# Performance work log

Hardware: AMD Instinct MI355X
Metric: run time of the kernel (lower is better)

The kernel has to match this reference:

```python
import jax, jax.numpy as jnp
import numpy as np

H = 16; W = 16; C_IN = 32; RNN_IN = 64; HID = 128; OUT = 512; B = 512


def _upsample_bilinear_ac(x, oh, ow):
    """Bilinear upsample with align_corners=True (matches nn.UpsamplingBilinear2d). x: (B,C,h,w)."""
    h, w = x.shape[2], x.shape[3]
    ys = (jnp.arange(oh, dtype=jnp.float32) * (h - 1) / (oh - 1))
    y0 = jnp.floor(ys).astype(jnp.int32)
    y1 = jnp.minimum(y0 + 1, h - 1)
    wy = (ys - y0.astype(jnp.float32))[None, None, :, None]
    xs = (jnp.arange(ow, dtype=jnp.float32) * (w - 1) / (ow - 1))
    x0 = jnp.floor(xs).astype(jnp.int32)
    x1 = jnp.minimum(x0 + 1, w - 1)
    wx = (xs - x0.astype(jnp.float32))[None, None, None, :]
    rows = x[:, :, y0, :] * (1.0 - wy) + x[:, :, y1, :] * wy  # (B,C,oh,w)
    out = rows[:, :, :, x0] * (1.0 - wx) + rows[:, :, :, x1] * wx  # (B,C,oh,ow)
    return out


def setup_inputs() -> dict:
    key = jax.random.key(0)
    ks = jax.random.split(key, 8)
    def winit(k, shape, fan_in):
        return jax.random.normal(k, shape, jnp.float32) / np.float32(np.sqrt(fan_in))
    return {
        "x": jax.random.normal(ks[0], (B, C_IN, H, W), jnp.float32),
        "h0": jax.random.normal(ks[1], (B, HID), jnp.float32),
        "W_in": winit(ks[2], (RNN_IN, C_IN), C_IN),
        "b_in": jnp.zeros((RNN_IN,), jnp.float32),
        "W_ih": winit(ks[3], (HID, RNN_IN), RNN_IN),
        "b_ih": jnp.zeros((HID,), jnp.float32),
        "W_hh": winit(ks[4], (HID, HID), HID),
        "b_hh": jnp.zeros((HID,), jnp.float32),
        "W_out": winit(ks[5], (OUT, HID), HID),
        "b_out": jnp.zeros((OUT,), jnp.float32),
    }


def reference(x, h0, W_in, b_in, W_ih, b_ih, W_hh, b_hh, W_out, b_out):
    b = x.shape[0]
    # (B,C,H,W) -> (B,L,C), L = H*W raster order
    x_seq = x.transpose(0, 2, 3, 1).reshape(b, H * W, C_IN)
    proj = x_seq @ W_in.T + b_in                      # (B,L,RNN_IN)
    pre = proj @ W_ih.T + b_ih                        # (B,L,HID), input part of RNNCell precomputed

    def step(h, p_t):
        h_new = jnp.tanh(p_t + h @ W_hh.T + b_hh)
        return h_new, h_new

    _, hs = jax.lax.scan(step, h0, pre.transpose(1, 0, 2))  # (L,B,HID)
    hs_map = hs.reshape(H, W, b, HID).transpose(2, 3, 0, 1)  # (B,HID,H,W)
    up = _upsample_bilinear_ac(hs_map, 2 * H, 2 * W)         # (B,HID,32,32)
    act = up * jnp.clip(up + 3.0, 0.0, 6.0) * (1.0 / 6.0)    # hardswish
    pooled = act.mean(axis=(2, 3))                           # (B,HID)
    return pooled @ W_out.T + b_out
```

## Files before the change

### kernel.cpp

```cpp
#include <hip/hip_runtime.h>

#define L 256
#define BATCH 512
#define CIN 32
#define HIDN 128
#define OUTN 512

typedef _Float16 f16x8 __attribute__((ext_vector_type(8)));
typedef float f32x4 __attribute__((ext_vector_type(4)));

#define MFMA16(a, b, c) __builtin_amdgcn_mfma_f32_16x16x32_f16(a, b, c, 0, 0, 0)

static __device__ __forceinline__ unsigned short f16b(_Float16 h) {
    unsigned short u; __builtin_memcpy(&u, &h, 2); return u;
}


__global__ __launch_bounds__(256) void prep_kernel(
    const float* __restrict__ W_in, const float* __restrict__ b_in,
    const float* __restrict__ W_ih, const float* __restrict__ b_ih,
    const float* __restrict__ b_hh, const float* __restrict__ Whh,
    unsigned short* __restrict__ Wh, unsigned short* __restrict__ Wl,
    unsigned short* __restrict__ Wch, unsigned short* __restrict__ Wcl,
    float* __restrict__ bpre)
{
    const int tid = threadIdx.x;
    __shared__ float win[64 * CIN];
    for (int i = tid; i < 64 * CIN; i += 256) win[i] = W_in[i];
    __syncthreads();
    if (tid < 128) {
        const int j = tid;
        float acc[CIN];
#pragma unroll
        for (int c = 0; c < CIN; ++c) acc[c] = 0.f;
        float bs = b_ih[j] + b_hh[j];
        for (int m = 0; m < 64; ++m) {
            float w = W_ih[j * 64 + m];
            bs += w * b_in[m];
#pragma unroll
            for (int c = 0; c < CIN; ++c) acc[c] += w * win[m * CIN + c];
        }
        bpre[j] = bs;
#pragma unroll
        for (int c = 0; c < CIN; ++c) {
            _Float16 h = (_Float16)acc[c];
            _Float16 l = (_Float16)(acc[c] - (float)h);
            Wch[j * CIN + c] = f16b(h);
            Wcl[j * CIN + c] = f16b(l);
        }
    } else {
        const int j = tid - 128;
        for (int k = 0; k < HIDN; k += 4) {
            float4 v = *(const float4*)(Whh + j * HIDN + k);
            float vv[4] = {v.x, v.y, v.z, v.w};
#pragma unroll
            for (int u = 0; u < 4; ++u) {
                _Float16 h = (_Float16)vv[u];
                _Float16 l = (_Float16)(vv[u] - (float)h);
                Wh[j * HIDN + k + u] = f16b(h);
                Wl[j * HIDN + k + u] = f16b(l);
            }
        }
    }
}

__global__ __launch_bounds__(512, 1) void rnn_kernel(
    const float* __restrict__ x, const float* __restrict__ h0,
    const unsigned short* __restrict__ Wh, const unsigned short* __restrict__ Wl,
    const unsigned short* __restrict__ Wch, const unsigned short* __restrict__ Wcl,
    const float* __restrict__ bpre, unsigned short* __restrict__ hs)
{
    const int tid = threadIdx.x;
    const int bb = blockIdx.x;
    const int lane = tid & 63;
    const int w = tid >> 6;
    const int n = lane & 15;
    const int q = lane >> 4;

    __shared__ unsigned short hbuf[2][16][HIDN];
    __shared__ unsigned short xc[2][16][16][CIN];

    f16x8 Ah[4], Al[4], Axh, Axl;
    const int jr = w * 16 + n;
#pragma unroll
    for (int kc = 0; kc < 4; ++kc) {
        Ah[kc] = *(const f16x8*)(Wh + jr * HIDN + kc * 32 + q * 8);
        Al[kc] = *(const f16x8*)(Wl + jr * HIDN + kc * 32 + q * 8);
    }
    Axh = *(const f16x8*)(Wch + jr * CIN + q * 8);
    Axl = *(const f16x8*)(Wcl + jr * CIN + q * 8);
    float4 bv = *(const float4*)(bpre + w * 16 + q * 4);
    f32x4 bp = (f32x4){bv.x, bv.y, bv.z, bv.w};

    if (tid < 256) {
        const int ni = tid >> 4, gi = tid & 15;
        const float4* src = (const float4*)(h0 + ((size_t)bb * 16 + ni) * HIDN + gi * 8);
        float4 a = src[0], b4 = src[1];
        float vv[8] = {a.x, a.y, a.z, a.w, b4.x, b4.y, b4.z, b4.w};
        unsigned short o[8];
#pragma unroll
        for (int i = 0; i < 8; ++i) o[i] = f16b((_Float16)vv[i]);
        *(uint4*)&hbuf[0][ni][(gi ^ (ni & 7)) * 8] = *(uint4*)o;
    }

    float4 xr[4];
    auto issue_chunk = [&](int ci) {
#pragma unroll
        for (int r = 0; r < 4; ++r) {
            int i = tid + r * 512;
            int nn = i >> 7, cc = (i >> 2) & 31, tq = i & 3;
            xr[r] = *(const float4*)(x + (((size_t)bb * 16 + nn) * CIN + cc) * L + ci * 16 + tq * 4);
        }
    };
    auto write_chunk = [&](int buf) {
#pragma unroll
        for (int r = 0; r < 4; ++r) {
            int i = tid + r * 512;
            int nn = i >> 7, cc = (i >> 2) & 31, tq = i & 3;
            float vv[4] = {xr[r].x, xr[r].y, xr[r].z, xr[r].w};
#pragma unroll
            for (int k = 0; k < 4; ++k)
                xc[buf][tq * 4 + k][nn][cc] = f16b((_Float16)vv[k]);
        }
    };

    issue_chunk(0);
    write_chunk(0);
    issue_chunk(1);
    __syncthreads();

    unsigned short* hsp = hs + ((size_t)bb * 16 + n) * HIDN + w * 16 + q * 4;

    for (int t = 0; t < L; ++t) {
        const int p = t & 1;
        const int cb = (t >> 4) & 1, tt = t & 15;

        f16x8 Bh[4];
#pragma unroll
        for (int kc = 0; kc < 4; ++kc)
            Bh[kc] = *(const f16x8*)&hbuf[p][n][((4 * kc + q) ^ (n & 7)) * 8];
        f16x8 xB = *(const f16x8*)&xc[cb][tt][n][q * 8];

        f32x4 aH = bp;
        f32x4 aL = (f32x4){0.f, 0.f, 0.f, 0.f};
#pragma unroll
        for (int kc = 0; kc < 4; ++kc) {
            aH = MFMA16(Ah[kc], Bh[kc], aH);
            aL = MFMA16(Al[kc], Bh[kc], aL);
        }
        aH = MFMA16(Axh, xB, aH);
        aL = MFMA16(Axl, xB, aL);

        if (tt == 15 && t < L - 16) {
            write_chunk(cb ^ 1);
            if (t < L - 32) issue_chunk((t >> 4) + 2);
        }

        f32x4 acc = aH + aL;
        unsigned short o[4];
#pragma unroll
        for (int r = 0; r < 4; ++r) {
            float e = __expf(2.f * acc[r]);
            float hv = 1.f - 2.f * __builtin_amdgcn_rcpf(e + 1.f);
            o[r] = f16b((_Float16)hv);
        }
        uint2 pk; __builtin_memcpy(&pk, o, 8);
        const int G = (w * 2 + (q >> 1)) ^ (n & 7);
        *(uint2*)&hbuf[p ^ 1][n][G * 8 + (q & 1) * 4] = pk;
        *(uint2*)(hsp + (size_t)t * (BATCH * HIDN)) = pk;

        asm volatile("" ::: "memory");
        __builtin_amdgcn_s_waitcnt(0xC07F);
        __builtin_amdgcn_s_barrier();
        asm volatile("" ::: "memory");
    }
}

__global__ __launch_bounds__(256) void pool_out_kernel(
    const unsigned short* __restrict__ hs, const float* __restrict__ W_out,
    const float* __restrict__ b_out, float* __restrict__ out)
{
    const int b = blockIdx.x, tid = threadIdx.x;
    __shared__ unsigned short m[L][HIDN];
    __shared__ float ps[2][HIDN];
    __shared__ float pooled_s[HIDN];

#pragma unroll
    for (int it = 0; it < 16; ++it) {
        int i = tid + it * 256;
        int t = i >> 4, g = i & 15;
        *(uint4*)&m[t][g * 8] =
            *(const uint4*)(hs + (size_t)t * (BATCH * HIDN) + b * HIDN + g * 8);
    }
    __syncthreads();

    const int jo = tid & 127, sub = tid >> 7;
    float acc = 0.f;
    for (int oy = sub * 16; oy < sub * 16 + 16; ++oy) {
        float ysf = oy * (15.f / 31.f);
        int y0 = (int)ysf; float wy = ysf - (float)y0; int y1 = min(y0 + 1, 15);
        float rb[16];
#pragma unroll
        for (int sx = 0; sx < 16; ++sx) {
            float v0 = (float)*(const _Float16*)&m[y0 * 16 + sx][jo];
            float v1 = (float)*(const _Float16*)&m[y1 * 16 + sx][jo];
            rb[sx] = v0 + wy * (v1 - v0);
        }
#pragma unroll
        for (int ox = 0; ox < 32; ++ox) {
            float xsf = ox * (15.f / 31.f);
            int x0 = (int)xsf; float wx = xsf - (float)x0; int x1 = min(x0 + 1, 15);
            float v = rb[x0] + wx * (rb[x1] - rb[x0]);
            float t6 = fminf(fmaxf(v + 3.f, 0.f), 6.f);
            acc += v * t6;
        }
    }
    ps[sub][jo] = acc;
    __syncthreads();
    if (tid < 128) pooled_s[tid] = (ps[0][tid] + ps[1][tid]) * (1.f / 6144.f);
    __syncthreads();

    for (int o = tid; o < OUTN; o += 256) {
        float a = b_out[o];
#pragma unroll 8
        for (int k = 0; k < HIDN; k += 4) {
            float4 wv = *(const float4*)(W_out + o * HIDN + k);
            float4 pv = *(const float4*)&pooled_s[k];
            a += wv.x * pv.x + wv.y * pv.y + wv.z * pv.z + wv.w * pv.w;
        }
        out[b * OUTN + o] = a;
    }
}

extern "C" void kernel_launch(void* const* d_in, const int* in_sizes, int n_in,
                              void* d_out, int out_size, void* d_ws, size_t ws_size,
                              hipStream_t stream)
{
    const float* x     = (const float*)d_in[0];
    const float* h0    = (const float*)d_in[1];
    const float* W_in  = (const float*)d_in[2];
    const float* b_in  = (const float*)d_in[3];
    const float* W_ih  = (const float*)d_in[4];
    const float* b_ih  = (const float*)d_in[5];
    const float* W_hh  = (const float*)d_in[6];
    const float* b_hh  = (const float*)d_in[7];
    const float* W_out = (const float*)d_in[8];
    const float* b_out = (const float*)d_in[9];
    float* out = (float*)d_out;

    char* wsb = (char*)d_ws;
    unsigned short* Wh  = (unsigned short*)(wsb);
    unsigned short* Wl  = (unsigned short*)(wsb + 32768);
    unsigned short* Wch = (unsigned short*)(wsb + 65536);
    unsigned short* Wcl = (unsigned short*)(wsb + 73728);
    float* bpre         = (float*)(wsb + 81920);
    unsigned short* hsb = (unsigned short*)(wsb + 98304);

    prep_kernel<<<1, 256, 0, stream>>>(W_in, b_in, W_ih, b_ih, b_hh, W_hh,
                                       Wh, Wl, Wch, Wcl, bpre);
    rnn_kernel<<<32, 512, 0, stream>>>(x, h0, Wh, Wl, Wch, Wcl, bpre, hsb);
    pool_out_kernel<<<512, 256, 0, stream>>>(hsb, W_out, b_out, out);
}
```

Baseline: 228.3 us.

## Pretranspose x to fp16 in prep kernel and shorten recurrent MFMA chain

Adds 32 extra blocks to the prep kernel that transpose x into a time-major fp16 layout in workspace. The RNN kernel can then fetch each step's input directly with a one-step-ahead register prefetch, replacing the shared-memory chunk staging that ran every 16 steps. The per-step MFMA dependency chain is split across four accumulators so the sequential recurrence has lower latency, and the loop is unrolled by two. The cost is an extra global round trip for x and a prefetch that reads one step past the end of the buffer.

New measurement: 245.1 us. +7.3%, slower.

```diff
diff --git a/kernel.cpp b/kernel.cpp
--- a/kernel.cpp
+++ b/kernel.cpp
@@ -17,14 +17,51 @@
 
 
 __global__ __launch_bounds__(256) void prep_kernel(
+    const float* __restrict__ x,
     const float* __restrict__ W_in, const float* __restrict__ b_in,
     const float* __restrict__ W_ih, const float* __restrict__ b_ih,
     const float* __restrict__ b_hh, const float* __restrict__ Whh,
     unsigned short* __restrict__ Wh, unsigned short* __restrict__ Wl,
     unsigned short* __restrict__ Wch, unsigned short* __restrict__ Wcl,
-    float* __restrict__ bpre)
+    float* __restrict__ bpre, unsigned short* __restrict__ xT)
 {
     const int tid = threadIdx.x;
+
+    if (blockIdx.x != 0) {
+        const int bb = blockIdx.x - 1;
+        __shared__ float tile[32][16][33];
+        const int wv = tid >> 6, l = tid & 63;
+        const int wn = l >> 2, wc0 = (l & 3) * 8;
+        for (int tc = 0; tc < 8; ++tc) {
+#pragma unroll
+            for (int r = 0; r < 16; ++r) {
+                int i = tid + r * 256;
+                int nn = i >> 8, cc = (i >> 3) & 31, tq = i & 7;
+                float4 v = *(const float4*)(
+                    x + ((size_t)(bb * 16 + nn) * CIN + cc) * L + tc * 32 + tq * 4);
+                int cs = cc ^ ((tq & 3) << 3);
+                tile[tq * 4 + 0][nn][cs] = v.x;
+                tile[tq * 4 + 1][nn][cs] = v.y;
+                tile[tq * 4 + 2][nn][cs] = v.z;
+                tile[tq * 4 + 3][nn][cs] = v.w;
+            }
+            __syncthreads();
+#pragma unroll
+            for (int it = 0; it < 8; ++it) {
+                int tl = wv + it * 4;
+                int swz = ((tl >> 2) & 3) << 3;
+                const float* src = &tile[tl][wn][wc0 ^ swz];
+                unsigned short o[8];
+#pragma unroll
+                for (int k = 0; k < 8; ++k) o[k] = f16b((_Float16)src[k]);
+                *(uint4*)(xT + ((size_t)(tc * 32 + tl) * BATCH + bb * 16 + wn) * CIN + wc0)
+                    = *(uint4*)o;
+            }
+            __syncthreads();
+        }
+        return;
+    }
+
     __shared__ float win[64 * CIN];
     for (int i = tid; i < 64 * CIN; i += 256) win[i] = W_in[i];
     __syncthreads();
@@ -44,9 +81,9 @@
 #pragma unroll
         for (int c = 0; c < CIN; ++c) {
             _Float16 h = (_Float16)acc[c];
-            _Float16 l = (_Float16)(acc[c] - (float)h);
+            _Float16 lo = (_Float16)(acc[c] - (float)h);
             Wch[j * CIN + c] = f16b(h);
-            Wcl[j * CIN + c] = f16b(l);
+            Wcl[j * CIN + c] = f16b(lo);
         }
     } else {
         const int j = tid - 128;
@@ -56,19 +93,20 @@
 #pragma unroll
             for (int u = 0; u < 4; ++u) {
                 _Float16 h = (_Float16)vv[u];
-                _Float16 l = (_Float16)(vv[u] - (float)h);
+                _Float16 lo = (_Float16)(vv[u] - (float)h);
                 Wh[j * HIDN + k + u] = f16b(h);
-                Wl[j * HIDN + k + u] = f16b(l);
+                Wl[j * HIDN + k + u] = f16b(lo);
             }
         }
     }
 }
 
 __global__ __launch_bounds__(512, 1) void rnn_kernel(
-    const float* __restrict__ x, const float* __restrict__ h0,
+    const float* __restrict__ h0,
     const unsigned short* __restrict__ Wh, const unsigned short* __restrict__ Wl,
     const unsigned short* __restrict__ Wch, const unsigned short* __restrict__ Wcl,
-    const float* __restrict__ bpre, unsigned short* __restrict__ hs)
+    const float* __restrict__ bpre, const unsigned short* __restrict__ xT,
+    unsigned short* __restrict__ hs)
 {
     const int tid = threadIdx.x;
     const int bb = blockIdx.x;
@@ -78,7 +116,6 @@
     const int q = lane >> 4;
 
     __shared__ unsigned short hbuf[2][16][HIDN];
-    __shared__ unsigned short xc[2][16][16][CIN];
 
     f16x8 Ah[4], Al[4], Axh, Axl;
     const int jr = w * 16 + n;
@@ -91,6 +128,11 @@
     Axl = *(const f16x8*)(Wcl + jr * CIN + q * 8);
     float4 bv = *(const float4*)(bpre + w * 16 + q * 4);
     f32x4 bp = (f32x4){bv.x, bv.y, bv.z, bv.w};
+    const f32x4 zero4 = (f32x4){0.f, 0.f, 0.f, 0.f};
+
+    const unsigned short* xp = xT + ((size_t)(bb * 16 + n) * CIN + q * 8);
+    f16x8 xb0, xb1;
+    xb0 = *(const f16x8*)(xp);
 
     if (tid < 256) {
         const int ni = tid >> 4, gi = tid & 15;
@@ -102,78 +144,50 @@
         for (int i = 0; i < 8; ++i) o[i] = f16b((_Float16)vv[i]);
         *(uint4*)&hbuf[0][ni][(gi ^ (ni & 7)) * 8] = *(uint4*)o;
     }
-
-    float4 xr[4];
-    auto issue_chunk = [&](int ci) {
-#pragma unroll
-        for (int r = 0; r < 4; ++r) {
-            int i = tid + r * 512;
-            int nn = i >> 7, cc = (i >> 2) & 31, tq = i & 3;
-            xr[r] = *(const float4*)(x + (((size_t)bb * 16 + nn) * CIN + cc) * L + ci * 16 + tq * 4);
-        }
-    };
-    auto write_chunk = [&](int buf) {
-#pragma unroll
-        for (int r = 0; r < 4; ++r) {
-            int i = tid + r * 512;
-            int nn = i >> 7, cc = (i >> 2) & 31, tq = i & 3;
-            float vv[4] = {xr[r].x, xr[r].y, xr[r].z, xr[r].w};
-#pragma unroll
-            for (int k = 0; k < 4; ++k)
-                xc[buf][tq * 4 + k][nn][cc] = f16b((_Float16)vv[k]);
-        }
-    };
-
-    issue_chunk(0);
-    write_chunk(0);
-    issue_chunk(1);
     __syncthreads();
 
     unsigned short* hsp = hs + ((size_t)bb * 16 + n) * HIDN + w * 16 + q * 4;
-
-    for (int t = 0; t < L; ++t) {
-        const int p = t & 1;
-        const int cb = (t >> 4) & 1, tt = t & 15;
-
-        f16x8 Bh[4];
-#pragma unroll
-        for (int kc = 0; kc < 4; ++kc)
-            Bh[kc] = *(const f16x8*)&hbuf[p][n][((4 * kc + q) ^ (n & 7)) * 8];
-        f16x8 xB = *(const f16x8*)&xc[cb][tt][n][q * 8];
-
-        f32x4 aH = bp;
-        f32x4 aL = (f32x4){0.f, 0.f, 0.f, 0.f};
-#pragma unroll
-        for (int kc = 0; kc < 4; ++kc) {
-            aH = MFMA16(Ah[kc], Bh[kc], aH);
-            aL = MFMA16(Al[kc], Bh[kc], aL);
-        }
-        aH = MFMA16(Axh, xB, aH);
-        aL = MFMA16(Axl, xB, aL);
-
-        if (tt == 15 && t < L - 16) {
-            write_chunk(cb ^ 1);
-            if (t < L - 32) issue_chunk((t >> 4) + 2);
-        }
-
-        f32x4 acc = aH + aL;
-        unsigned short o[4];
-#pragma unroll
-        for (int r = 0; r < 4; ++r) {
-            float e = __expf(2.f * acc[r]);
-            float hv = 1.f - 2.f * __builtin_amdgcn_rcpf(e + 1.f);
-            o[r] = f16b((_Float16)hv);
-        }
-        uint2 pk; __builtin_memcpy(&pk, o, 8);
-        const int G = (w * 2 + (q >> 1)) ^ (n & 7);
-        *(uint2*)&hbuf[p ^ 1][n][G * 8 + (q & 1) * 4] = pk;
-        *(uint2*)(hsp + (size_t)t * (BATCH * HIDN)) = pk;
-
-        asm volatile("" ::: "memory");
-        __builtin_amdgcn_s_waitcnt(0xC07F);
-        __builtin_amdgcn_s_barrier();
-        asm volatile("" ::: "memory");
-    }
+    const int G = (w * 2 + (q >> 1)) ^ (n & 7);
+    const int sw = n & 7;
+
+#define STEP(T, IN, OUT, XCUR, XNEXT)                                          \
+    {                                                                          \
+        XNEXT = *(const f16x8*)(xp + (size_t)((T) + 1) * (BATCH * CIN));       \
+        f16x8 Bh0 = *(const f16x8*)&hbuf[IN][n][((0 + q) ^ sw) * 8];           \
+        f16x8 Bh1 = *(const f16x8*)&hbuf[IN][n][((4 + q) ^ sw) * 8];           \
+        f16x8 Bh2 = *(const f16x8*)&hbuf[IN][n][((8 + q) ^ sw) * 8];           \
+        f16x8 Bh3 = *(const f16x8*)&hbuf[IN][n][((12 + q) ^ sw) * 8];          \
+        f32x4 c0 = MFMA16(Axh, XCUR, bp);                                      \
+        f32x4 c2 = MFMA16(Axl, XCUR, zero4);                                   \
+        c0 = MFMA16(Ah[0], Bh0, c0);                                           \
+        c2 = MFMA16(Al[0], Bh0, c2);                                           \
+        f32x4 c1 = MFMA16(Ah[1], Bh1, zero4);                                  \
+        f32x4 c3 = MFMA16(Al[1], Bh1, zero4);                                  \
+        c0 = MFMA16(Ah[2], Bh2, c0);                                           \
+        c2 = MFMA16(Al[2], Bh2, c2);                                           \
+        c1 = MFMA16(Ah[3], Bh3, c1);                                           \
+        c3 = MFMA16(Al[3], Bh3, c3);                                           \
+        f32x4 acc = (c0 + c1) + (c2 + c3);                                     \
+        unsigned short o[4];                                                   \
+        for (int r = 0; r < 4; ++r) {                                          \
+            float e = __expf(2.f * acc[r]);                                    \
+            float hv = 1.f - 2.f * __builtin_amdgcn_rcpf(e + 1.f);             \
+            o[r] = f16b((_Float16)hv);                                         \
+        }                                                                      \
+        uint2 pk; __builtin_memcpy(&pk, o, 8);                                 \
+        *(uint2*)&hbuf[OUT][n][G * 8 + (q & 1) * 4] = pk;                      \
+        *(uint2*)(hsp + (size_t)(T) * (BATCH * HIDN)) = pk;                    \
+        asm volatile("" ::: "memory");                                         \
+        __builtin_amdgcn_s_waitcnt(0xC07F);               \
+        __builtin_amdgcn_s_barrier();                                          \
+        asm volatile("" ::: "memory");                                         \
+    }
+
+    for (int t = 0; t < L; t += 2) {
+        STEP(t,     0, 1, xb0, xb1);
+        STEP(t + 1, 1, 0, xb1, xb0);
+    }
+#undef STEP
 }
 
 __global__ __launch_bounds__(256) void pool_out_kernel(
@@ -255,9 +269,10 @@
     unsigned short* Wcl = (unsigned short*)(wsb + 73728);
     float* bpre         = (float*)(wsb + 81920);
     unsigned short* hsb = (unsigned short*)(wsb + 98304);
-
-    prep_kernel<<<1, 256, 0, stream>>>(W_in, b_in, W_ih, b_ih, b_hh, W_hh,
-                                       Wh, Wl, Wch, Wcl, bpre);
-    rnn_kernel<<<32, 512, 0, stream>>>(x, h0, Wh, Wl, Wch, Wcl, bpre, hsb);
+    unsigned short* xT  = (unsigned short*)(wsb + 33652736);
+
+    prep_kernel<<<33, 256, 0, stream>>>(x, W_in, b_in, W_ih, b_ih, b_hh, W_hh,
+                                        Wh, Wl, Wch, Wcl, bpre, xT);
+    rnn_kernel<<<32, 512, 0, stream>>>(h0, Wh, Wl, Wch, Wcl, bpre, xT, hsb);
     pool_out_kernel<<<512, 256, 0, stream>>>(hsb, W_out, b_out, out);
 }
```

## Restructure RNN step: split MFMA chains, prefetch x operand, swizzle x LDS layout

Applied to the files above, without the earlier changes.

Unrolls the recurrent loop by two with compile-time ping-pong buffers. The dependent MFMA chain is split into four shorter accumulator chains, and the input-projection MFMA is issued first so it does not wait on the hidden state. The next step's x operand is loaded from LDS before the barrier, and the waitcnt is relaxed so that load can stay in flight. The x chunk is stored in a swizzled layout to avoid bank conflicts, and the chunk write is moved one step earlier so the prefetched value sees fresh data. The aim is lower per-step latency on the serial critical path, at the cost of more registers and some risk of ordering bugs around the early x load.

New measurement: 217.1 us. -4.9%, faster.

```diff
diff --git a/kernel.cpp b/kernel.cpp
--- a/kernel.cpp
+++ b/kernel.cpp
@@ -78,7 +78,7 @@
     const int q = lane >> 4;
 
     __shared__ unsigned short hbuf[2][16][HIDN];
-    __shared__ unsigned short xc[2][16][16][CIN];
+    __shared__ unsigned short xcl[2][16][64][8];
 
     f16x8 Ah[4], Al[4], Axh, Axl;
     const int jr = w * 16 + n;
@@ -91,6 +91,7 @@
     Axl = *(const f16x8*)(Wcl + jr * CIN + q * 8);
     float4 bv = *(const float4*)(bpre + w * 16 + q * 4);
     f32x4 bp = (f32x4){bv.x, bv.y, bv.z, bv.w};
+    const f32x4 zero4 = (f32x4){0.f, 0.f, 0.f, 0.f};
 
     if (tid < 256) {
         const int ni = tid >> 4, gi = tid & 15;
@@ -117,10 +118,11 @@
         for (int r = 0; r < 4; ++r) {
             int i = tid + r * 512;
             int nn = i >> 7, cc = (i >> 2) & 31, tq = i & 3;
+            int gr = (cc >> 3) * 16 + (nn ^ ((cc >> 3) << 2));
             float vv[4] = {xr[r].x, xr[r].y, xr[r].z, xr[r].w};
 #pragma unroll
             for (int k = 0; k < 4; ++k)
-                xc[buf][tq * 4 + k][nn][cc] = f16b((_Float16)vv[k]);
+                xcl[buf][tq * 4 + k][gr][cc & 7] = f16b((_Float16)vv[k]);
         }
     };
 
@@ -130,50 +132,56 @@
     __syncthreads();
 
     unsigned short* hsp = hs + ((size_t)bb * 16 + n) * HIDN + w * 16 + q * 4;
-
-    for (int t = 0; t < L; ++t) {
-        const int p = t & 1;
-        const int cb = (t >> 4) & 1, tt = t & 15;
-
-        f16x8 Bh[4];
-#pragma unroll
-        for (int kc = 0; kc < 4; ++kc)
-            Bh[kc] = *(const f16x8*)&hbuf[p][n][((4 * kc + q) ^ (n & 7)) * 8];
-        f16x8 xB = *(const f16x8*)&xc[cb][tt][n][q * 8];
-
-        f32x4 aH = bp;
-        f32x4 aL = (f32x4){0.f, 0.f, 0.f, 0.f};
-#pragma unroll
-        for (int kc = 0; kc < 4; ++kc) {
-            aH = MFMA16(Ah[kc], Bh[kc], aH);
-            aL = MFMA16(Al[kc], Bh[kc], aL);
-        }
-        aH = MFMA16(Axh, xB, aH);
-        aL = MFMA16(Axl, xB, aL);
-
-        if (tt == 15 && t < L - 16) {
-            write_chunk(cb ^ 1);
-            if (t < L - 32) issue_chunk((t >> 4) + 2);
-        }
-
-        f32x4 acc = aH + aL;
-        unsigned short o[4];
-#pragma unroll
-        for (int r = 0; r < 4; ++r) {
-            float e = __expf(2.f * acc[r]);
-            float hv = 1.f - 2.f * __builtin_amdgcn_rcpf(e + 1.f);
-            o[r] = f16b((_Float16)hv);
-        }
-        uint2 pk; __builtin_memcpy(&pk, o, 8);
-        const int G = (w * 2 + (q >> 1)) ^ (n & 7);
-        *(uint2*)&hbuf[p ^ 1][n][G * 8 + (q & 1) * 4] = pk;
-        *(uint2*)(hsp + (size_t)t * (BATCH * HIDN)) = pk;
-
-        asm volatile("" ::: "memory");
-        __builtin_amdgcn_s_waitcnt(0xC07F);
-        __builtin_amdgcn_s_barrier();
-        asm volatile("" ::: "memory");
-    }
+    const int G = (w * 2 + (q >> 1)) ^ (n & 7);
+    const int sw = n & 7;
+    const int grs = q * 16 + (n ^ (q << 2));
+
+    f16x8 xb0, xb1;
+    xb0 = *(const f16x8*)&xcl[0][0][grs][0];
+
+#define STEP(T, IN, OUT, OFF, XCUR, XNEXT)                                     \
+    {                                                                          \
+        f16x8 Bh0 = *(const f16x8*)&hbuf[IN][n][((0 + q) ^ sw) * 8];           \
+        f16x8 Bh1 = *(const f16x8*)&hbuf[IN][n][((4 + q) ^ sw) * 8];           \
+        f16x8 Bh2 = *(const f16x8*)&hbuf[IN][n][((8 + q) ^ sw) * 8];           \
+        f16x8 Bh3 = *(const f16x8*)&hbuf[IN][n][((12 + q) ^ sw) * 8];          \
+        f32x4 c0 = MFMA16(Axh, XCUR, bp);            \
+        f32x4 c2 = MFMA16(Axl, XCUR, zero4);                                   \
+        c0 = MFMA16(Ah[0], Bh0, c0);                                           \
+        c2 = MFMA16(Al[0], Bh0, c2);                                           \
+        f32x4 c1 = MFMA16(Ah[1], Bh1, zero4);                                  \
+        f32x4 c3 = MFMA16(Al[1], Bh1, zero4);                                  \
+        c0 = MFMA16(Ah[2], Bh2, c0);                                           \
+        c2 = MFMA16(Al[2], Bh2, c2);                                           \
+        c1 = MFMA16(Ah[3], Bh3, c1);                                           \
+        c3 = MFMA16(Al[3], Bh3, c3);                                           \
+        if (((T) & 15) == 14 && (T) < L - 16) {                                \
+            write_chunk((((T) >> 4) & 1) ^ 1);                                 \
+            if ((T) < L - 32) issue_chunk(((T) >> 4) + 2);                     \
+        }                                                                      \
+        f32x4 acc = (c0 + c1) + (c2 + c3);                                     \
+        unsigned short o[4];                                                   \
+        for (int r = 0; r < 4; ++r) {                                          \
+            float e = __expf(2.f * acc[r]);                                    \
+            float hv = 1.f - 2.f * __builtin_amdgcn_rcpf(e + 1.f);             \
+            o[r] = f16b((_Float16)hv);                                         \
+        }                                                                      \
+        uint2 pk; __builtin_memcpy(&pk, o, 8);                                 \
+        *(uint2*)&hbuf[OUT][n][G * 8 + (q & 1) * 4] = pk;                      \
+        *(uint2*)(hsp + (OFF)) = pk;                                           \
+        XNEXT = *(const f16x8*)&xcl[(((T) + 1) >> 4) & 1][((T) + 1) & 15][grs][0]; \
+        asm volatile("" ::: "memory");                                         \
+        __builtin_amdgcn_s_waitcnt(0xC17F);   \
+        __builtin_amdgcn_s_barrier();         \
+        asm volatile("" ::: "memory");                                         \
+    }
+
+    for (int t = 0; t < L; t += 2) {
+        STEP(t,     0, 1, 0,             xb0, xb1);
+        STEP(t + 1, 1, 0, BATCH * HIDN,  xb1, xb0);
+        hsp += 2 * (BATCH * HIDN);
+    }
+#undef STEP
 }
 
 __global__ __launch_bounds__(256) void pool_out_kernel(
```
